# Optimization experiments

Measured on AMD Instinct MI355X. Metric: run time of the kernel, lower is better.

Reference implementation:

```python
import jax, jax.numpy as jnp
import numpy as np


def setup_inputs() -> dict:
    key = jax.random.key(0)
    k1, k2 = jax.random.split(key)
    B, Lq, Ls, D = 16, 2048, 2048, 512
    query = jax.random.normal(k1, (B, Lq, D), dtype=jnp.float32)
    support = jax.random.normal(k2, (B, Ls, D), dtype=jnp.float32)
    return {"query": query, "support": support}


def reference(query, support):
    # attn: [B, Lq, Ls] = softmax(query @ support^T, axis=-1)
    logits = jnp.einsum("bqd,bsd->bqs", query, support)
    attn = jax.nn.softmax(logits, axis=-1)
    # attended support: [B, Lq, D]
    attended = jnp.einsum("bqs,bsd->bqd", attn, support)
    # score: [B, Lq] = sum over D of query * attended
    score = jnp.sum(query * attended, axis=-1)
    return score
```

## Files before the change

### kernel.cpp

```cpp
#include <hip/hip_runtime.h>
#include <hip/hip_bf16.h>

#define B_  16
#define LQ  2048
#define LS  2048
#define DD  512
#define BQ  256
#define BS  256
#define BK  64
#define NSB (LS / BS)
#define NKC (DD / BK)
#define NSPLIT 4

static_assert(NKC == 8, "stage>>3 math assumes NKC==8");

typedef short bf16x8 __attribute__((ext_vector_type(8)));
typedef float f32x4  __attribute__((ext_vector_type(4)));

__device__ __forceinline__ void load_lds16(const void* g, void* l) {
  __builtin_amdgcn_global_load_lds((const __attribute__((address_space(1))) void*)g,
                                   (__attribute__((address_space(3))) void*)l,
                                   16, 0, 0);
}

__device__ __forceinline__ unsigned short f2bf(float f) {
  union { float f; unsigned int u; } v; v.f = f;
  unsigned int r = v.u + 0x7fffu + ((v.u >> 16) & 1u);
  return (unsigned short)(r >> 16);
}

__global__ __launch_bounds__(256) void cvt_kernel(const float* __restrict__ Q,
                                                  const float* __restrict__ S,
                                                  unsigned short* __restrict__ Qw,
                                                  unsigned short* __restrict__ Sw) {
  const int half = gridDim.x >> 1;
  int blk = blockIdx.x;
  const float* src; unsigned short* dst;
  if (blk < half) { src = Q; dst = Qw; } else { src = S; dst = Sw; blk -= half; }
  const size_t n4 = (size_t)B_ * LQ * DD / 4;
  const size_t stride = (size_t)half * 256;
  for (size_t i = (size_t)blk * 256 + threadIdx.x; i < n4; i += stride) {
    float4 f = ((const float4*)src)[i];
    ushort4 u;
    u.x = f2bf(f.x); u.y = f2bf(f.y); u.z = f2bf(f.z); u.w = f2bf(f.w);
    ((ushort4*)dst)[i] = u;
  }
}

__global__ __launch_bounds__(512, 2) void attn_kernel(const unsigned short* __restrict__ Qw,
                                                      const unsigned short* __restrict__ Sw,
                                                      float* __restrict__ out,
                                                      float* __restrict__ pm,
                                                      float* __restrict__ pse,
                                                      float* __restrict__ psel,
                                                      int nsplit) {
  __shared__ __align__(16) unsigned short sQ[2][BQ * BK];
  __shared__ __align__(16) unsigned short sS[2][BS * BK];

  const int pid = blockIdx.x + (blockIdx.y << 3) + (blockIdx.z << 7);
  const int nch = (nsplit << 7) >> 3;
  const int lid = (pid & 7) * nch + (pid >> 3);
  const int qb   = lid & 7;
  const int rest = lid >> 3;
  const int spl  = rest & (nsplit - 1);
  const int b    = rest >> (nsplit == 4 ? 2 : 0);

  const int tid  = threadIdx.x;
  const int w    = tid >> 6;
  const int lane = tid & 63;
  const int h    = w & 1;
  const int g    = w >> 1;
  const int col  = lane & 15;
  const int quad = lane >> 4;
  const int c7   = col & 7;

  const int q0 = qb * BQ;
  const unsigned short* Qb = Qw + (size_t)b * LQ * DD;
  const unsigned short* Sb = Sw + (size_t)b * LS * DD;

  float mst[4] = { -INFINITY, -INFINITY, -INFINITY, -INFINITY };
  float se[4]  = { 0.f, 0.f, 0.f, 0.f };
  float sel[4] = { 0.f, 0.f, 0.f, 0.f };

  f32x4 acc[8][4];
#pragma unroll
  for (int st = 0; st < 8; ++st)
#pragma unroll
    for (int qt = 0; qt < 4; ++qt)
      acc[st][qt] = (f32x4){0.f, 0.f, 0.f, 0.f};

  const int rr = lane >> 3;
  const int cc = ((lane & 7) ^ rr) * 8;

  const int sbs = spl * (NSB / nsplit);
  const int nst = (NSB / nsplit) * NKC;

  auto issue_stage = [&](int t_i, int buf) {
    const int kc = t_i & 7;
    if (w < 4) {
      const unsigned short* gp = Qb + (size_t)(q0 + w * 64 + rr) * DD + kc * BK + cc;
      unsigned short* lp = &sQ[buf][(w * 64) * BK];
#pragma unroll
      for (int i = 0; i < 8; ++i)
        load_lds16(gp + (size_t)i * 8 * DD, lp + i * 8 * BK);
    } else {
      const int sb = sbs + (t_i >> 3);
      const unsigned short* gp = Sb + (size_t)(sb * BS + (w - 4) * 64 + rr) * DD + kc * BK + cc;
      unsigned short* lp = &sS[buf][((w - 4) * 64) * BK];
#pragma unroll
      for (int i = 0; i < 8; ++i)
        load_lds16(gp + (size_t)i * 8 * DD, lp + i * 8 * BK);
    }
  };

  issue_stage(0, 0);
  asm volatile("s_waitcnt vmcnt(0)" ::: "memory");
  __builtin_amdgcn_s_barrier();
  __builtin_amdgcn_sched_barrier(0);
  int cur = 0;

#pragma unroll 1
  for (int t = 0; t < nst; ++t) {
    const int tn = t + 1;
    if (tn < nst) issue_stage(tn, cur ^ 1);

    const unsigned short* bq = &sQ[cur][0];
    const unsigned short* bs = &sS[cur][0];
    __builtin_amdgcn_s_setprio(1);
#pragma unroll
    for (int kk = 0; kk < 2; ++kk) {
      const int koff = ((kk * 4 + quad) ^ c7) * 8;
      bf16x8 asv[8];
#pragma unroll
      for (int st = 0; st < 8; ++st)
        asv[st] = *(const bf16x8*)&bs[(h * 128 + st * 16 + col) * BK + koff];
#pragma unroll
      for (int qt = 0; qt < 4; ++qt) {
        bf16x8 aq = *(const bf16x8*)&bq[(g * 64 + qt * 16 + col) * BK + koff];
#pragma unroll
        for (int st = 0; st < 8; ++st)
          acc[st][qt] = __builtin_amdgcn_mfma_f32_16x16x32_bf16(asv[st], aq, acc[st][qt], 0, 0, 0);
      }
    }
    __builtin_amdgcn_s_setprio(0);

    asm volatile("s_waitcnt vmcnt(0)" ::: "memory");
    __builtin_amdgcn_s_barrier();
    __builtin_amdgcn_sched_barrier(0);
    cur ^= 1;

    if ((t & (NKC - 1)) == NKC - 1) {
#pragma unroll
      for (int qt = 0; qt < 4; ++qt) {
        float lmax = mst[qt];
#pragma unroll
        for (int st = 0; st < 8; ++st)
#pragma unroll
          for (int r = 0; r < 4; ++r)
            lmax = fmaxf(lmax, acc[st][qt][r]);
        lmax = fmaxf(lmax, __shfl_xor(lmax, 16, 64));
        lmax = fmaxf(lmax, __shfl_xor(lmax, 32, 64));
        float alpha = __expf(mst[qt] - lmax);
        float pe = 0.f, pel = 0.f;
#pragma unroll
        for (int st = 0; st < 8; ++st)
#pragma unroll
          for (int r = 0; r < 4; ++r) {
            float l = acc[st][qt][r];
            float e = __expf(l - lmax);
            pe += e;
            pel = fmaf(e, l, pel);
          }
        pe  += __shfl_xor(pe, 16, 64);  pe  += __shfl_xor(pe, 32, 64);
        pel += __shfl_xor(pel, 16, 64); pel += __shfl_xor(pel, 32, 64);
        se[qt]  = fmaf(se[qt],  alpha, pe);
        sel[qt] = fmaf(sel[qt], alpha, pel);
        mst[qt] = lmax;
#pragma unroll
        for (int st = 0; st < 8; ++st)
          acc[st][qt] = (f32x4){0.f, 0.f, 0.f, 0.f};
      }
    }
  }

  __syncthreads();
  float* red = (float*)&sQ[0][0];
  if (quad == 0) {
#pragma unroll
    for (int qt = 0; qt < 4; ++qt) {
      int qq = g * 64 + qt * 16 + col;
      red[h * 256 + qq]        = mst[qt];
      red[512 + h * 256 + qq]  = se[qt];
      red[1024 + h * 256 + qq] = sel[qt];
    }
  }
  __syncthreads();
  if (h == 0 && quad == 0) {
#pragma unroll
    for (int qt = 0; qt < 4; ++qt) {
      int qq = g * 64 + qt * 16 + col;
      float m0 = red[qq],       m1 = red[256 + qq];
      float M  = fmaxf(m0, m1);
      float a0 = __expf(m0 - M), a1 = __expf(m1 - M);
      float SE  = red[512 + qq]  * a0 + red[512 + 256 + qq]  * a1;
      float SEL = red[1024 + qq] * a0 + red[1024 + 256 + qq] * a1;
      size_t qi = (size_t)b * LQ + q0 + qq;
      if (nsplit == 1) {
        out[qi] = SEL / SE;
      } else {
        pm[qi * NSPLIT + spl]   = M;
        pse[qi * NSPLIT + spl]  = SE;
        psel[qi * NSPLIT + spl] = SEL;
      }
    }
  }
}

__global__ __launch_bounds__(256) void combine_kernel(const float* __restrict__ pm,
                                                      const float* __restrict__ pse,
                                                      const float* __restrict__ psel,
                                                      float* __restrict__ out) {
  int i = blockIdx.x * blockDim.x + threadIdx.x;
  if (i >= B_ * LQ) return;
  float M = -INFINITY;
#pragma unroll
  for (int s = 0; s < NSPLIT; ++s) M = fmaxf(M, pm[i * NSPLIT + s]);
  float SE = 0.f, SEL = 0.f;
#pragma unroll
  for (int s = 0; s < NSPLIT; ++s) {
    float a = __expf(pm[i * NSPLIT + s] - M);
    SE  = fmaf(pse[i * NSPLIT + s],  a, SE);
    SEL = fmaf(psel[i * NSPLIT + s], a, SEL);
  }
  out[i] = SEL / SE;
}

__global__ __launch_bounds__(256) void fallback_kernel(const float* __restrict__ Q,
                                                       const float* __restrict__ S,
                                                       float* __restrict__ out) {
  __shared__ float qv[DD];
  __shared__ float red[256];
  const int b = blockIdx.y, qi = blockIdx.x, tid = threadIdx.x;
  const float* qrow = Q + ((size_t)b * LQ + qi) * DD;
  for (int d = tid; d < DD; d += 256) qv[d] = qrow[d];
  __syncthreads();
  const float* Sb = S + (size_t)b * LS * DD;
  float m = -INFINITY, se = 0.f, sel = 0.f;
  for (int s = tid; s < LS; s += 256) {
    const float* srow = Sb + (size_t)s * DD;
    float dot = 0.f;
    for (int d = 0; d < DD; ++d) dot = fmaf(qv[d], srow[d], dot);
    float mn = fmaxf(m, dot);
    float a = __expf(m - mn);
    float e = __expf(dot - mn);
    se  = se * a + e;
    sel = sel * a + e * dot;
    m = mn;
  }
  red[tid] = m; __syncthreads();
  for (int o = 128; o > 0; o >>= 1) { if (tid < o) red[tid] = fmaxf(red[tid], red[tid + o]); __syncthreads(); }
  float M = red[0]; __syncthreads();
  float a = __expf(m - M); se *= a; sel *= a;
  red[tid] = se; __syncthreads();
  for (int o = 128; o > 0; o >>= 1) { if (tid < o) red[tid] += red[tid + o]; __syncthreads(); }
  float SE = red[0]; __syncthreads();
  red[tid] = sel; __syncthreads();
  for (int o = 128; o > 0; o >>= 1) { if (tid < o) red[tid] += red[tid + o]; __syncthreads(); }
  float SEL = red[0];
  if (tid == 0) out[(size_t)b * LQ + qi] = SEL / SE;
}

extern "C" void kernel_launch(void* const* d_in, const int* in_sizes, int n_in,
                              void* d_out, int out_size, void* d_ws, size_t ws_size,
                              hipStream_t stream) {
  const float* Q = (const float*)d_in[0];
  const float* S = (const float*)d_in[1];
  float* out = (float*)d_out;
  const size_t nelem = (size_t)B_ * LQ * DD;
  const size_t need_base  = 2 * nelem * sizeof(unsigned short);
  const size_t part_elems = (size_t)B_ * LQ * NSPLIT;
  const size_t need_split = need_base + 3 * part_elems * sizeof(float);

  if (ws_size >= need_base) {
    unsigned short* Qw = (unsigned short*)d_ws;
    unsigned short* Sw = Qw + nelem;
    cvt_kernel<<<2048, 256, 0, stream>>>(Q, S, Qw, Sw);
    if (ws_size >= need_split) {
      float* pm   = (float*)(Sw + nelem);
      float* pse  = pm + part_elems;
      float* psel = pse + part_elems;
      attn_kernel<<<dim3(LQ / BQ, B_, NSPLIT), 512, 0, stream>>>(Qw, Sw, out, pm, pse, psel, NSPLIT);
      combine_kernel<<<(B_ * LQ + 255) / 256, 256, 0, stream>>>(pm, pse, psel, out);
    } else {
      attn_kernel<<<dim3(LQ / BQ, B_, 1), 512, 0, stream>>>(Qw, Sw, out, nullptr, nullptr, nullptr, 1);
    }
  } else {
    fallback_kernel<<<dim3(LQ, B_), 256, 0, stream>>>(Q, S, out);
  }
}
```

Baseline: 217.7 us.

## Split K-stages into 32-wide halves with 4-slot LDS ring and prefetch depth 3

Replaces the double-buffered 64-wide K-chunk pipeline with a four-slot ring of 32-wide half-chunks, issuing loads three stages ahead and waiting with partial vmcnt counts instead of draining all loads each iteration. The barrier moves to the top of each step, giving one barrier per half-chunk. The LDS swizzle is changed to suit the 32-element rows, and MFMA issue is split into two groups of 16 with explicit lgkmcnt waits. The goal is to hide global-to-LDS latency better. The cost is twice as many barriers and smaller compute bursts between them.

```diff
diff --git a/kernel.cpp b/kernel.cpp
--- a/kernel.cpp
+++ b/kernel.cpp
@@ -8,6 +8,7 @@
 #define BQ  256
 #define BS  256
 #define BK  64
+#define HK  32
 #define NSB (LS / BS)
 #define NKC (DD / BK)
 #define NSPLIT 4
@@ -54,8 +55,8 @@
                                                       float* __restrict__ pse,
                                                       float* __restrict__ psel,
                                                       int nsplit) {
-  __shared__ __align__(16) unsigned short sQ[2][BQ * BK];
-  __shared__ __align__(16) unsigned short sS[2][BS * BK];
+  __shared__ __align__(16) unsigned short sQh[4][BQ * HK];
+  __shared__ __align__(16) unsigned short sSh[4][BS * HK];
 
   const int pid = blockIdx.x + (blockIdx.y << 3) + (blockIdx.z << 7);
   const int nch = (nsplit << 7) >> 3;
@@ -72,7 +73,6 @@
   const int g    = w >> 1;
   const int col  = lane & 15;
   const int quad = lane >> 4;
-  const int c7   = col & 7;
 
   const int q0 = qb * BQ;
   const unsigned short* Qb = Qw + (size_t)b * LQ * DD;
@@ -89,67 +89,78 @@
     for (int qt = 0; qt < 4; ++qt)
       acc[st][qt] = (f32x4){0.f, 0.f, 0.f, 0.f};
 
-  const int rr = lane >> 3;
-  const int cc = ((lane & 7) ^ rr) * 8;
+  const int cc8 = (((lane & 3) ^ ((lane >> 2) & 3)) * 8);
+  const int rl  = lane >> 2;
+  const int koq = ((quad ^ (col & 3)) * 8);
 
   const int sbs = spl * (NSB / nsplit);
   const int nst = (NSB / nsplit) * NKC;
-
-  auto issue_stage = [&](int t_i, int buf) {
-    const int kc = t_i & 7;
+  const int U   = nst * 2;
+
+  auto issue_half = [&](int u) {
+    const int t  = u >> 1;
+    const int k0 = (t & 7) * 64 + (u & 1) * 32;
+    const int slot = u & 3;
     if (w < 4) {
-      const unsigned short* gp = Qb + (size_t)(q0 + w * 64 + rr) * DD + kc * BK + cc;
-      unsigned short* lp = &sQ[buf][(w * 64) * BK];
-#pragma unroll
-      for (int i = 0; i < 8; ++i)
-        load_lds16(gp + (size_t)i * 8 * DD, lp + i * 8 * BK);
+      const unsigned short* gp = Qb + (size_t)(q0 + w * 64 + rl) * DD + k0 + cc8;
+      unsigned short* lp = &sQh[slot][(w * 64) * HK];
+#pragma unroll
+      for (int i = 0; i < 4; ++i)
+        load_lds16(gp + (size_t)i * 16 * DD, lp + i * 16 * HK);
     } else {
-      const int sb = sbs + (t_i >> 3);
-      const unsigned short* gp = Sb + (size_t)(sb * BS + (w - 4) * 64 + rr) * DD + kc * BK + cc;
-      unsigned short* lp = &sS[buf][((w - 4) * 64) * BK];
-#pragma unroll
-      for (int i = 0; i < 8; ++i)
-        load_lds16(gp + (size_t)i * 8 * DD, lp + i * 8 * BK);
+      const int sb = sbs + (t >> 3);
+      const unsigned short* gp = Sb + (size_t)(sb * BS + (w - 4) * 64 + rl) * DD + k0 + cc8;
+      unsigned short* lp = &sSh[slot][((w - 4) * 64) * HK];
+#pragma unroll
+      for (int i = 0; i < 4; ++i)
+        load_lds16(gp + (size_t)i * 16 * DD, lp + i * 16 * HK);
     }
   };
 
-  issue_stage(0, 0);
-  asm volatile("s_waitcnt vmcnt(0)" ::: "memory");
-  __builtin_amdgcn_s_barrier();
-  __builtin_amdgcn_sched_barrier(0);
-  int cur = 0;
+  issue_half(0); issue_half(1); issue_half(2);
 
 #pragma unroll 1
-  for (int t = 0; t < nst; ++t) {
-    const int tn = t + 1;
-    if (tn < nst) issue_stage(tn, cur ^ 1);
-
-    const unsigned short* bq = &sQ[cur][0];
-    const unsigned short* bs = &sS[cur][0];
+  for (int u = 0; u < U; ++u) {
+    if (u < U - 2)       asm volatile("s_waitcnt vmcnt(8)" ::: "memory");
+    else if (u == U - 2) asm volatile("s_waitcnt vmcnt(4)" ::: "memory");
+    else                 asm volatile("s_waitcnt vmcnt(0)" ::: "memory");
+    __builtin_amdgcn_s_barrier();
+    if (u + 3 < U) issue_half(u + 3);
+
+    const unsigned short* bq = &sQh[u & 3][0];
+    const unsigned short* bs = &sSh[u & 3][0];
+
+    bf16x8 aq[4], asv[4];
+#pragma unroll
+    for (int qt = 0; qt < 4; ++qt)
+      aq[qt] = *(const bf16x8*)&bq[(g * 64 + qt * 16 + col) * HK + koq];
+#pragma unroll
+    for (int st = 0; st < 4; ++st)
+      asv[st] = *(const bf16x8*)&bs[(h * 128 + st * 16 + col) * HK + koq];
+    asm volatile("s_waitcnt lgkmcnt(0)" ::: "memory");
+    __builtin_amdgcn_sched_barrier(0);
     __builtin_amdgcn_s_setprio(1);
 #pragma unroll
-    for (int kk = 0; kk < 2; ++kk) {
-      const int koff = ((kk * 4 + quad) ^ c7) * 8;
-      bf16x8 asv[8];
-#pragma unroll
-      for (int st = 0; st < 8; ++st)
-        asv[st] = *(const bf16x8*)&bs[(h * 128 + st * 16 + col) * BK + koff];
-#pragma unroll
-      for (int qt = 0; qt < 4; ++qt) {
-        bf16x8 aq = *(const bf16x8*)&bq[(g * 64 + qt * 16 + col) * BK + koff];
-#pragma unroll
-        for (int st = 0; st < 8; ++st)
-          acc[st][qt] = __builtin_amdgcn_mfma_f32_16x16x32_bf16(asv[st], aq, acc[st][qt], 0, 0, 0);
-      }
-    }
+    for (int qt = 0; qt < 4; ++qt)
+#pragma unroll
+      for (int st = 0; st < 4; ++st)
+        acc[st][qt] = __builtin_amdgcn_mfma_f32_16x16x32_bf16(asv[st], aq[qt], acc[st][qt], 0, 0, 0);
     __builtin_amdgcn_s_setprio(0);
 
-    asm volatile("s_waitcnt vmcnt(0)" ::: "memory");
-    __builtin_amdgcn_s_barrier();
+#pragma unroll
+    for (int st = 0; st < 4; ++st)
+      asv[st] = *(const bf16x8*)&bs[(h * 128 + (4 + st) * 16 + col) * HK + koq];
+    asm volatile("s_waitcnt lgkmcnt(0)" ::: "memory");
     __builtin_amdgcn_sched_barrier(0);
-    cur ^= 1;
-
-    if ((t & (NKC - 1)) == NKC - 1) {
+    __builtin_amdgcn_s_setprio(1);
+#pragma unroll
+    for (int qt = 0; qt < 4; ++qt)
+#pragma unroll
+      for (int st = 0; st < 4; ++st)
+        acc[4 + st][qt] = __builtin_amdgcn_mfma_f32_16x16x32_bf16(asv[st], aq[qt], acc[4 + st][qt], 0, 0, 0);
+    __builtin_amdgcn_s_setprio(0);
+
+    if ((u & (2 * NKC - 1)) == 2 * NKC - 1) {
 #pragma unroll
       for (int qt = 0; qt < 4; ++qt) {
         float lmax = mst[qt];
@@ -184,7 +195,7 @@
   }
 
   __syncthreads();
-  float* red = (float*)&sQ[0][0];
+  float* red = (float*)&sQh[0][0];
   if (quad == 0) {
 #pragma unroll
     for (int qt = 0; qt < 4; ++qt) {
```

New measurement: 222.7 us. +2.3%, slower.
